# Kernel tuning notes

Measured on AMD Instinct MI355X. Metric: run time of the kernel, lower is better.

Reference implementation:

```python
import jax, jax.numpy as jnp
import numpy as np

B, S, D_MODEL, D_OUT = 4, 4096, 512, 64


def setup_inputs() -> dict:
    key = jax.random.key(0)
    ks = jax.random.split(key, 10)
    query = jax.random.normal(ks[0], (B, S, D_MODEL), dtype=jnp.float32)
    key_t = jax.random.normal(ks[1], (B, S, D_MODEL), dtype=jnp.float32)
    value = jax.random.normal(ks[2], (B, S, D_MODEL), dtype=jnp.float32)
    mask = jax.random.randint(ks[3], (B, S, S), 0, 2, dtype=jnp.int32)
    sc = 1.0 / np.sqrt(D_MODEL)
    Wq = jax.random.uniform(ks[4], (D_MODEL, D_OUT), minval=-sc, maxval=sc, dtype=jnp.float32)
    bq = jnp.zeros((D_OUT,), dtype=jnp.float32)
    Wk = jax.random.uniform(ks[5], (D_MODEL, D_OUT), minval=-sc, maxval=sc, dtype=jnp.float32)
    bk = jnp.zeros((D_OUT,), dtype=jnp.float32)
    Wv = jax.random.uniform(ks[6], (D_MODEL, D_OUT), minval=-sc, maxval=sc, dtype=jnp.float32)
    bv = jnp.zeros((D_OUT,), dtype=jnp.float32)
    return {"query": query, "key": key_t, "value": value, "mask": mask,
            "Wq": Wq, "bq": bq, "Wk": Wk, "bk": bk, "Wv": Wv, "bv": bv}


def reference(query, key, value, mask, Wq, bq, Wk, bk, Wv, bv):
    # Linear projections (single head): [B,S,D_MODEL] @ [D_MODEL,D_OUT] + bias
    q = jnp.einsum('bsd,de->bse', query, Wq) + bq
    k = jnp.einsum('bsd,de->bse', key, Wk) + bk
    v = jnp.einsum('bsd,de->bse', value, Wv) + bv
    dim_k = k.shape[-1]
    scores = jnp.einsum('bqe,bke->bqk', q, k) / jnp.sqrt(jnp.float32(dim_k))  # [B,S,S]
    scores = jnp.where(mask == 0, -jnp.inf, scores)
    weights = jax.nn.softmax(scores, axis=-1)
    # dropout is identity in eval mode / for deterministic reference
    outputs = jnp.einsum('bqk,bke->bqe', weights, v)  # [B,S,D_OUT]
    return outputs
```

## Files before the change

kernel.cpp:

```cpp
#include <hip/hip_runtime.h>
#include <hip/hip_bf16.h>

#define BB 4
#define SS 4096
#define DMODEL 512
#define DOUT 64
#define NKH 2
#define KH (SS / NKH)
#define NIT (KH / 64)

typedef __bf16 bf16_t;
typedef __bf16 bf16x8 __attribute__((ext_vector_type(8)));
typedef float floatx4 __attribute__((ext_vector_type(4)));
typedef unsigned long long u64;
typedef u64 u64x2 __attribute__((ext_vector_type(2)));

__device__ inline void gl_lds16(const void* g, void* l) {
  __builtin_amdgcn_global_load_lds(
      (const __attribute__((address_space(1))) unsigned int*)g,
      (__attribute__((address_space(3))) unsigned int*)l, 16, 0, 0);
}

__global__ __launch_bounds__(256) void wtrans_kernel(
    const float* __restrict__ Wq, const float* __restrict__ Wk,
    const float* __restrict__ Wv, bf16_t* __restrict__ wT) {
  int idx = blockIdx.x * 256 + threadIdx.x;
  int mat = idx >> 12;
  int r   = idx & 4095;
  int e   = r & 63;
  int d0  = (r >> 6) << 3;
  const float* W = (mat == 0) ? Wq : ((mat == 1) ? Wk : Wv);
  bf16_t* dst = wT + (size_t)mat * (DOUT * DMODEL) + (size_t)e * DMODEL + d0;
#pragma unroll
  for (int j = 0; j < 8; ++j) dst[j] = (bf16_t)W[(size_t)(d0 + j) * DOUT + e];
}

__global__ __launch_bounds__(256) void maskpack_kernel(
    const int* __restrict__ mask, u64* __restrict__ bits) {
  const int wid  = (blockIdx.x * 256 + threadIdx.x) >> 6;
  const int lane = threadIdx.x & 63;
  const int* base = mask + (size_t)wid * 1024;
  u64* wbase = bits + (size_t)wid * 16;
#pragma unroll
  for (int c = 0; c < 4; ++c) {
    const int* p = base + c * 256;
    u64 b0 = __ballot(p[lane] != 0);
    u64 b1 = __ballot(p[lane + 64] != 0);
    u64 b2 = __ballot(p[lane + 128] != 0);
    u64 b3 = __ballot(p[lane + 192] != 0);
    u64x2 w01 = {b0, b1}, w23 = {b2, b3};
    if (lane == 0) *(u64x2*)(wbase + c * 4) = w01;
    if (lane == 1) *(u64x2*)(wbase + c * 4 + 2) = w23;
  }
}

__global__ __launch_bounds__(256) void proj_kernel(
    const float* __restrict__ inq, const float* __restrict__ ink,
    const float* __restrict__ inv, const bf16_t* __restrict__ wT,
    const float* __restrict__ bq, const float* __restrict__ bk,
    const float* __restrict__ bv,
    bf16_t* __restrict__ q_ws, bf16_t* __restrict__ k_ws,
    bf16_t* __restrict__ v_wsT) {
  const int mat = blockIdx.x >> 8;
  const int s0  = (blockIdx.x & 255) << 6;
  const int lane = threadIdx.x & 63;
  const int w    = threadIdx.x >> 6;
  const int col  = lane & 15, quad = lane >> 4;

  const float* inp  = (mat == 0) ? inq : ((mat == 1) ? ink : inv);
  const float* bias = (mat == 0) ? bq : ((mat == 1) ? bk : bv);
  const bf16_t* wt  = wT + (size_t)mat * (DOUT * DMODEL);

  const int arow = s0 + w * 16 + col;
  floatx4 acc[4] = {};

  for (int ch = 0; ch < 16; ++ch) {
    const int d0 = ch * 32 + quad * 8;
    float4 a0 = *(const float4*)(inp + (size_t)arow * DMODEL + d0);
    float4 a1 = *(const float4*)(inp + (size_t)arow * DMODEL + d0 + 4);
    bf16x8 af;
    af[0] = (bf16_t)a0.x; af[1] = (bf16_t)a0.y; af[2] = (bf16_t)a0.z; af[3] = (bf16_t)a0.w;
    af[4] = (bf16_t)a1.x; af[5] = (bf16_t)a1.y; af[6] = (bf16_t)a1.z; af[7] = (bf16_t)a1.w;
#pragma unroll
    for (int c = 0; c < 4; ++c) {
      bf16x8 bw = *(const bf16x8*)(wt + (size_t)(c * 16 + col) * DMODEL + d0);
      acc[c] = __builtin_amdgcn_mfma_f32_16x16x32_bf16(af, bw, acc[c], 0, 0, 0);
    }
  }

#pragma unroll
  for (int c = 0; c < 4; ++c) {
    float bcol = bias[c * 16 + col];
#pragma unroll
    for (int r = 0; r < 4; ++r) {
      int row = s0 + w * 16 + quad * 4 + r;
      float v = acc[c][r] + bcol;
      if (mat == 2) {
        int b = row >> 12, sp = row & 4095;
        v_wsT[((size_t)(b * DOUT + c * 16 + col)) * SS + sp] = (bf16_t)v;
      } else {
        bf16_t* dst = (mat == 0) ? q_ws : k_ws;
        dst[(size_t)row * DOUT + c * 16 + col] = (bf16_t)v;
      }
    }
  }
}

__global__ __launch_bounds__(256, 2) void attn_kernel(
    const bf16_t* __restrict__ q_ws, const bf16_t* __restrict__ k_ws,
    const bf16_t* __restrict__ v_wsT, const u64* __restrict__ bits,
    float* __restrict__ O_part, float* __restrict__ l_part) {
  const int bq = blockIdx.x >> 1, kh = blockIdx.x & 1;
  const int b  = bq >> 6;
  const int q0 = (bq & 63) << 6;
  const int kbase = kh * KH;
  const int lane = threadIdx.x & 63;
  const int wi   = threadIdx.x >> 6;
  const int col  = lane & 15, quad = lane >> 4;

  __shared__ __align__(16) bf16_t Kb[2][64 * 64];
  __shared__ __align__(16) bf16_t Vb[2][64 * 64];
  __shared__ __align__(16) bf16_t Pl[4][16][72];

  const int qrowA = q0 + wi * 16 + col;
  const bf16_t* qbase = q_ws + ((size_t)(b * SS) + qrowA) * DOUT + quad * 8;
  const bf16x8 qa0 = *(const bf16x8*)(qbase);
  const bf16x8 qa1 = *(const bf16x8*)(qbase + 32);
  const u64* brow = bits + ((size_t)(b * SS) + qrowA) * (SS / 64);

  const int srow = lane >> 3;
  const int schk = (lane & 7) ^ srow;

  auto stage = [&](int it, int buf) {
    const int k0 = kbase + it * 64;
#pragma unroll
    for (int j = 0; j < 2; ++j) {
      const int i = wi * 2 + j;
      const int r = i * 8 + srow;
      const char* gK = (const char*)(k_ws + ((size_t)(b * SS) + k0 + r) * DOUT) + schk * 16;
      gl_lds16(gK, (char*)(&Kb[buf][0]) + i * 1024);
      const char* gV = (const char*)(v_wsT + ((size_t)(b * DOUT) + r) * SS + k0) + schk * 16;
      gl_lds16(gV, (char*)(&Vb[buf][0]) + i * 1024);
    }
  };

  floatx4 o[4] = {};
  float l_acc = 0.f;
  const bf16_t* prow_r = &Pl[wi][col][quad * 8];

  stage(0, 0);
  u64 bits_cur = brow[kbase >> 6];
  __syncthreads();

  for (int it = 0; it < NIT; ++it) {
    const int buf = it & 1;
    const int itn = (it + 1 < NIT) ? it + 1 : it;

    stage(itn, buf ^ 1);
    u64 bits_nxt = brow[(kbase + itn * 64) >> 6];

    floatx4 sacc[4];
#pragma unroll
    for (int c = 0; c < 4; ++c) {
      const int row = c * 16 + col;
      bf16x8 k0f = *(const bf16x8*)((const char*)&Kb[buf][0] + row * 128 + ((quad ^ (col & 7)) * 16));
      bf16x8 k1f = *(const bf16x8*)((const char*)&Kb[buf][0] + row * 128 + (((4 | quad) ^ (col & 7)) * 16));
      floatx4 z = {};
      z = __builtin_amdgcn_mfma_f32_16x16x32_bf16(qa0, k0f, z, 0, 0, 0);
      z = __builtin_amdgcn_mfma_f32_16x16x32_bf16(qa1, k1f, z, 0, 0, 0);
      sacc[c] = z;
    }

    bf16x8 vc[4][2];
#pragma unroll
    for (int c = 0; c < 4; ++c) {
      const int row = c * 16 + col;
      vc[c][0] = *(const bf16x8*)((const char*)&Vb[buf][0] + row * 128 + ((quad ^ (col & 7)) * 16));
      vc[c][1] = *(const bf16x8*)((const char*)&Vb[buf][0] + row * 128 + (((4 | quad) ^ (col & 7)) * 16));
    }

#pragma unroll
    for (int c = 0; c < 4; ++c)
#pragma unroll
      for (int r = 0; r < 4; ++r)
        Pl[wi][quad * 4 + r][c * 16 + col] = (bf16_t)__expf(sacc[c][r] * 0.125f);

    asm volatile("s_waitcnt lgkmcnt(0)" ::: "memory");

    bf16x8 pa0 = *(const bf16x8*)(prow_r);
    bf16x8 pa1 = *(const bf16x8*)(prow_r + 32);

    unsigned lo32 = (unsigned)bits_cur;
    unsigned hi32 = (unsigned)(bits_cur >> 32);
    unsigned m8a = (lo32 >> (quad * 8)) & 0xffu;
    unsigned m8b = (hi32 >> (quad * 8)) & 0xffu;
    float lp = 0.f;
    bf16x8 pm0, pm1;
#pragma unroll
    for (int j = 0; j < 8; ++j) {
      bf16_t p0 = ((m8a >> j) & 1u) ? pa0[j] : (bf16_t)0.0f;
      bf16_t p1 = ((m8b >> j) & 1u) ? pa1[j] : (bf16_t)0.0f;
      pm0[j] = p0; pm1[j] = p1;
      lp += (float)p0 + (float)p1;
    }
    lp += __shfl_xor(lp, 16);
    lp += __shfl_xor(lp, 32);
    l_acc += lp;

#pragma unroll
    for (int c = 0; c < 4; ++c) {
      o[c] = __builtin_amdgcn_mfma_f32_16x16x32_bf16(pm0, vc[c][0], o[c], 0, 0, 0);
      o[c] = __builtin_amdgcn_mfma_f32_16x16x32_bf16(pm1, vc[c][1], o[c], 0, 0, 0);
    }

    bits_cur = bits_nxt;
    __syncthreads();
  }

  float* Op = O_part + (size_t)blockIdx.x * 64 * 64;
#pragma unroll
  for (int c = 0; c < 4; ++c)
#pragma unroll
    for (int r = 0; r < 4; ++r)
      Op[(wi * 16 + quad * 4 + r) * 64 + c * 16 + col] = o[c][r];
  if (quad == 0) l_part[(size_t)blockIdx.x * 64 + wi * 16 + col] = l_acc;
}

__global__ __launch_bounds__(256) void combine_kernel(
    const float* __restrict__ O_part, const float* __restrict__ l_part,
    float* __restrict__ out) {
  const int idx = blockIdx.x * 256 + threadIdx.x;
  const int base = idx * 4;
  const int row = base >> 6;
  const int c   = base & 63;
  const int t   = row >> 6;
  const int rl  = row & 63;
  const float* p0 = O_part + (((size_t)(t * 2 + 0) * 64 + rl) * 64 + c);
  const float* p1 = O_part + (((size_t)(t * 2 + 1) * 64 + rl) * 64 + c);
  const float inv = 1.0f / (l_part[(size_t)(t * 2) * 64 + rl] +
                            l_part[(size_t)(t * 2 + 1) * 64 + rl]);
  float4 a = *(const float4*)p0;
  float4 b = *(const float4*)p1;
  float4 r4 = {(a.x + b.x) * inv, (a.y + b.y) * inv,
               (a.z + b.z) * inv, (a.w + b.w) * inv};
  *(float4*)(out + base) = r4;
}

extern "C" void kernel_launch(void* const* d_in, const int* in_sizes, int n_in,
                              void* d_out, int out_size, void* d_ws, size_t ws_size,
                              hipStream_t stream) {
  const float* query = (const float*)d_in[0];
  const float* key   = (const float*)d_in[1];
  const float* value = (const float*)d_in[2];
  const int*   mask  = (const int*)d_in[3];
  const float* Wq = (const float*)d_in[4];
  const float* bq = (const float*)d_in[5];
  const float* Wk = (const float*)d_in[6];
  const float* bk = (const float*)d_in[7];
  const float* Wv = (const float*)d_in[8];
  const float* bv = (const float*)d_in[9];
  float* out = (float*)d_out;

  bf16_t* q_ws  = (bf16_t*)d_ws;
  bf16_t* k_ws  = q_ws + (size_t)BB * SS * DOUT;
  bf16_t* v_wsT = k_ws + (size_t)BB * SS * DOUT;
  bf16_t* wT    = v_wsT + (size_t)BB * SS * DOUT;
  float*  O_part = (float*)(wT + 3 * DOUT * DMODEL);
  float*  l_part = O_part + (size_t)512 * 64 * 64;
  u64*    bits   = (u64*)(l_part + 512 * 64);

  hipLaunchKernelGGL(maskpack_kernel, dim3(BB * SS * SS / 1024 / 4), dim3(256), 0, stream,
                     mask, bits);
  hipLaunchKernelGGL(wtrans_kernel, dim3(48), dim3(256), 0, stream, Wq, Wk, Wv, wT);
  hipLaunchKernelGGL(proj_kernel, dim3(768), dim3(256), 0, stream,
                     query, key, value, wT, bq, bk, bv, q_ws, k_ws, v_wsT);
  hipLaunchKernelGGL(attn_kernel, dim3(512), dim3(256), 0, stream,
                     q_ws, k_ws, v_wsT, bits, O_part, l_part);
  hipLaunchKernelGGL(combine_kernel, dim3(1024), dim3(256), 0, stream,
                     O_part, l_part, out);
}
```

Measured before the change: 499.8 us.

## Double query tile per block and split keys four ways

Each attention block now handles 128 query rows (32 per wave) instead of 64, so every K/V tile staged in LDS is reused across twice as many queries. The key range is split into four chunks instead of two, which keeps the grid at 512 blocks, and the combine kernel sums four partials. The MFMA operands are swapped so the score layout lets each lane write a packed bf16x4 of masked probabilities, with masking applied before the LDS write. Register pressure rises because each wave holds twice as many accumulators, and the partial buffers grow.

```diff
diff --git a/kernel.cpp b/kernel.cpp
--- a/kernel.cpp
+++ b/kernel.cpp
@@ -5,11 +5,13 @@
 #define SS 4096
 #define DMODEL 512
 #define DOUT 64
-#define NKH 2
+#define NKH 4
 #define KH (SS / NKH)
-#define NIT (KH / 64)
+#define BK 64
+#define NIT (KH / BK)
 
 typedef __bf16 bf16_t;
+typedef __bf16 bf16x4 __attribute__((ext_vector_type(4)));
 typedef __bf16 bf16x8 __attribute__((ext_vector_type(8)));
 typedef float floatx4 __attribute__((ext_vector_type(4)));
 typedef unsigned long long u64;
@@ -110,46 +112,52 @@
     const bf16_t* __restrict__ q_ws, const bf16_t* __restrict__ k_ws,
     const bf16_t* __restrict__ v_wsT, const u64* __restrict__ bits,
     float* __restrict__ O_part, float* __restrict__ l_part) {
-  const int bq = blockIdx.x >> 1, kh = blockIdx.x & 1;
-  const int b  = bq >> 6;
-  const int q0 = (bq & 63) << 6;
+  const int kh = blockIdx.x & 3;
+  const int qt = (blockIdx.x >> 2) & 31;
+  const int b  = blockIdx.x >> 7;
+  const int q0 = qt * 128;
   const int kbase = kh * KH;
   const int lane = threadIdx.x & 63;
   const int wi   = threadIdx.x >> 6;
   const int col  = lane & 15, quad = lane >> 4;
 
-  __shared__ __align__(16) bf16_t Kb[2][64 * 64];
-  __shared__ __align__(16) bf16_t Vb[2][64 * 64];
-  __shared__ __align__(16) bf16_t Pl[4][16][72];
-
-  const int qrowA = q0 + wi * 16 + col;
-  const bf16_t* qbase = q_ws + ((size_t)(b * SS) + qrowA) * DOUT + quad * 8;
-  const bf16x8 qa0 = *(const bf16x8*)(qbase);
-  const bf16x8 qa1 = *(const bf16x8*)(qbase + 32);
-  const u64* brow = bits + ((size_t)(b * SS) + qrowA) * (SS / 64);
+  __shared__ __align__(16) bf16_t Kb[2][BK * 64];
+  __shared__ __align__(16) bf16_t Vb[2][64 * BK];
+  __shared__ __align__(16) bf16_t Pl[4][32][72];
+
+  bf16x8 qa[2][2];
+#pragma unroll
+  for (int qg = 0; qg < 2; ++qg) {
+    const int qrow = q0 + wi * 32 + qg * 16 + col;
+    const bf16_t* qb = q_ws + ((size_t)(b * SS) + qrow) * DOUT + quad * 8;
+    qa[qg][0] = *(const bf16x8*)(qb);
+    qa[qg][1] = *(const bf16x8*)(qb + 32);
+  }
+  const u64* brow0 = bits + ((size_t)(b * SS) + q0 + wi * 32 + col) * (SS / 64);
+  const u64* brow1 = brow0 + (size_t)16 * (SS / 64);
 
   const int srow = lane >> 3;
   const int schk = (lane & 7) ^ srow;
 
   auto stage = [&](int it, int buf) {
-    const int k0 = kbase + it * 64;
+    const int k0 = kbase + it * BK;
 #pragma unroll
     for (int j = 0; j < 2; ++j) {
       const int i = wi * 2 + j;
       const int r = i * 8 + srow;
-      const char* gK = (const char*)(k_ws + ((size_t)(b * SS) + k0 + r) * DOUT) + schk * 16;
-      gl_lds16(gK, (char*)(&Kb[buf][0]) + i * 1024);
-      const char* gV = (const char*)(v_wsT + ((size_t)(b * DOUT) + r) * SS + k0) + schk * 16;
-      gl_lds16(gV, (char*)(&Vb[buf][0]) + i * 1024);
+      gl_lds16((const char*)(k_ws + ((size_t)(b * SS) + k0 + r) * DOUT) + schk * 16,
+               (char*)(&Kb[buf][0]) + i * 1024);
+      gl_lds16((const char*)(v_wsT + ((size_t)(b * DOUT) + r) * SS + k0) + schk * 16,
+               (char*)(&Vb[buf][0]) + i * 1024);
     }
   };
 
-  floatx4 o[4] = {};
-  float l_acc = 0.f;
-  const bf16_t* prow_r = &Pl[wi][col][quad * 8];
+  floatx4 o[2][4] = {};
+  float lacc[2] = {0.f, 0.f};
 
   stage(0, 0);
-  u64 bits_cur = brow[kbase >> 6];
+  u64 w0c = brow0[kh * NIT + 0];
+  u64 w1c = brow1[kh * NIT + 0];
   __syncthreads();
 
   for (int it = 0; it < NIT; ++it) {
@@ -157,73 +165,84 @@
     const int itn = (it + 1 < NIT) ? it + 1 : it;
 
     stage(itn, buf ^ 1);
-    u64 bits_nxt = brow[(kbase + itn * 64) >> 6];
-
-    floatx4 sacc[4];
+    u64 w0n = brow0[kh * NIT + itn];
+    u64 w1n = brow1[kh * NIT + itn];
+
+    floatx4 st[4][2];
+#pragma unroll
+    for (int kt = 0; kt < 4; ++kt) {
+      const int row = kt * 16 + col;
+      bf16x8 kf0 = *(const bf16x8*)((const char*)&Kb[buf][0] + row * 128 + ((quad ^ (col & 7)) * 16));
+      bf16x8 kf1 = *(const bf16x8*)((const char*)&Kb[buf][0] + row * 128 + (((4 | quad) ^ (col & 7)) * 16));
+#pragma unroll
+      for (int qg = 0; qg < 2; ++qg) {
+        floatx4 z = {};
+        z = __builtin_amdgcn_mfma_f32_16x16x32_bf16(kf0, qa[qg][0], z, 0, 0, 0);
+        z = __builtin_amdgcn_mfma_f32_16x16x32_bf16(kf1, qa[qg][1], z, 0, 0, 0);
+        st[kt][qg] = z;
+      }
+    }
+
+    bf16x8 vf[4][2];
 #pragma unroll
     for (int c = 0; c < 4; ++c) {
       const int row = c * 16 + col;
-      bf16x8 k0f = *(const bf16x8*)((const char*)&Kb[buf][0] + row * 128 + ((quad ^ (col & 7)) * 16));
-      bf16x8 k1f = *(const bf16x8*)((const char*)&Kb[buf][0] + row * 128 + (((4 | quad) ^ (col & 7)) * 16));
-      floatx4 z = {};
-      z = __builtin_amdgcn_mfma_f32_16x16x32_bf16(qa0, k0f, z, 0, 0, 0);
-      z = __builtin_amdgcn_mfma_f32_16x16x32_bf16(qa1, k1f, z, 0, 0, 0);
-      sacc[c] = z;
-    }
-
-    bf16x8 vc[4][2];
-#pragma unroll
-    for (int c = 0; c < 4; ++c) {
-      const int row = c * 16 + col;
-      vc[c][0] = *(const bf16x8*)((const char*)&Vb[buf][0] + row * 128 + ((quad ^ (col & 7)) * 16));
-      vc[c][1] = *(const bf16x8*)((const char*)&Vb[buf][0] + row * 128 + (((4 | quad) ^ (col & 7)) * 16));
-    }
-
+      vf[c][0] = *(const bf16x8*)((const char*)&Vb[buf][0] + row * 128 + ((quad ^ (col & 7)) * 16));
+      vf[c][1] = *(const bf16x8*)((const char*)&Vb[buf][0] + row * 128 + (((4 | quad) ^ (col & 7)) * 16));
+    }
+
+#pragma unroll
+    for (int qg = 0; qg < 2; ++qg) {
+      const u64 w = qg ? w1c : w0c;
+#pragma unroll
+      for (int kt = 0; kt < 4; ++kt) {
+        const unsigned nib = (unsigned)(w >> (kt * 16 + quad * 4)) & 0xfu;
+        float p[4];
+#pragma unroll
+        for (int r = 0; r < 4; ++r) {
+          float e = __expf(st[kt][qg][r] * 0.125f);
+          p[r] = (nib >> r & 1u) ? e : 0.0f;
+          lacc[qg] += p[r];
+        }
+        bf16x4 pk = {(bf16_t)p[0], (bf16_t)p[1], (bf16_t)p[2], (bf16_t)p[3]};
+        *(bf16x4*)(&Pl[wi][qg * 16 + col][kt * 16 + quad * 4]) = pk;
+      }
+    }
+
+    asm volatile("s_waitcnt lgkmcnt(0)" ::: "memory");
+
+    bf16x8 pf[2][2];
+#pragma unroll
+    for (int qg = 0; qg < 2; ++qg) {
+      pf[qg][0] = *(const bf16x8*)(&Pl[wi][qg * 16 + col][quad * 8]);
+      pf[qg][1] = *(const bf16x8*)(&Pl[wi][qg * 16 + col][32 + quad * 8]);
+    }
 #pragma unroll
     for (int c = 0; c < 4; ++c)
 #pragma unroll
-      for (int r = 0; r < 4; ++r)
-        Pl[wi][quad * 4 + r][c * 16 + col] = (bf16_t)__expf(sacc[c][r] * 0.125f);
-
-    asm volatile("s_waitcnt lgkmcnt(0)" ::: "memory");
-
-    bf16x8 pa0 = *(const bf16x8*)(prow_r);
-    bf16x8 pa1 = *(const bf16x8*)(prow_r + 32);
-
-    unsigned lo32 = (unsigned)bits_cur;
-    unsigned hi32 = (unsigned)(bits_cur >> 32);
-    unsigned m8a = (lo32 >> (quad * 8)) & 0xffu;
-    unsigned m8b = (hi32 >> (quad * 8)) & 0xffu;
-    float lp = 0.f;
-    bf16x8 pm0, pm1;
-#pragma unroll
-    for (int j = 0; j < 8; ++j) {
-      bf16_t p0 = ((m8a >> j) & 1u) ? pa0[j] : (bf16_t)0.0f;
-      bf16_t p1 = ((m8b >> j) & 1u) ? pa1[j] : (bf16_t)0.0f;
-      pm0[j] = p0; pm1[j] = p1;
-      lp += (float)p0 + (float)p1;
-    }
+      for (int qg = 0; qg < 2; ++qg) {
+        o[qg][c] = __builtin_amdgcn_mfma_f32_16x16x32_bf16(vf[c][0], pf[qg][0], o[qg][c], 0, 0, 0);
+        o[qg][c] = __builtin_amdgcn_mfma_f32_16x16x32_bf16(vf[c][1], pf[qg][1], o[qg][c], 0, 0, 0);
+      }
+
+    w0c = w0n; w1c = w1n;
+    __syncthreads();
+  }
+
+  float* Op = O_part + (size_t)blockIdx.x * 128 * 64;
+#pragma unroll
+  for (int qg = 0; qg < 2; ++qg) {
+    float lp = lacc[qg];
     lp += __shfl_xor(lp, 16);
     lp += __shfl_xor(lp, 32);
-    l_acc += lp;
-
+    const int rl = wi * 32 + qg * 16 + col;
+    if (quad == 0) l_part[(size_t)blockIdx.x * 128 + rl] = lp;
 #pragma unroll
     for (int c = 0; c < 4; ++c) {
-      o[c] = __builtin_amdgcn_mfma_f32_16x16x32_bf16(pm0, vc[c][0], o[c], 0, 0, 0);
-      o[c] = __builtin_amdgcn_mfma_f32_16x16x32_bf16(pm1, vc[c][1], o[c], 0, 0, 0);
-    }
-
-    bits_cur = bits_nxt;
-    __syncthreads();
-  }
-
-  float* Op = O_part + (size_t)blockIdx.x * 64 * 64;
-#pragma unroll
-  for (int c = 0; c < 4; ++c)
-#pragma unroll
-    for (int r = 0; r < 4; ++r)
-      Op[(wi * 16 + quad * 4 + r) * 64 + c * 16 + col] = o[c][r];
-  if (quad == 0) l_part[(size_t)blockIdx.x * 64 + wi * 16 + col] = l_acc;
+      float4 v = {o[qg][c][0], o[qg][c][1], o[qg][c][2], o[qg][c][3]};
+      *(float4*)(Op + (size_t)rl * 64 + c * 16 + quad * 4) = v;
+    }
+  }
 }
 
 __global__ __launch_bounds__(256) void combine_kernel(
@@ -233,16 +252,19 @@
   const int base = idx * 4;
   const int row = base >> 6;
   const int c   = base & 63;
-  const int t   = row >> 6;
-  const int rl  = row & 63;
-  const float* p0 = O_part + (((size_t)(t * 2 + 0) * 64 + rl) * 64 + c);
-  const float* p1 = O_part + (((size_t)(t * 2 + 1) * 64 + rl) * 64 + c);
-  const float inv = 1.0f / (l_part[(size_t)(t * 2) * 64 + rl] +
-                            l_part[(size_t)(t * 2 + 1) * 64 + rl]);
-  float4 a = *(const float4*)p0;
-  float4 b = *(const float4*)p1;
-  float4 r4 = {(a.x + b.x) * inv, (a.y + b.y) * inv,
-               (a.z + b.z) * inv, (a.w + b.w) * inv};
+  const int t   = row >> 7;
+  const int rl  = row & 127;
+  float4 acc = {0.f, 0.f, 0.f, 0.f};
+  float lsum = 0.f;
+#pragma unroll
+  for (int kh = 0; kh < NKH; ++kh) {
+    const size_t blk = (size_t)(t * NKH + kh);
+    float4 a = *(const float4*)(O_part + (blk * 128 + rl) * 64 + c);
+    acc.x += a.x; acc.y += a.y; acc.z += a.z; acc.w += a.w;
+    lsum += l_part[blk * 128 + rl];
+  }
+  const float inv = 1.0f / lsum;
+  float4 r4 = {acc.x * inv, acc.y * inv, acc.z * inv, acc.w * inv};
   *(float4*)(out + base) = r4;
 }
 
@@ -266,15 +288,15 @@
   bf16_t* v_wsT = k_ws + (size_t)BB * SS * DOUT;
   bf16_t* wT    = v_wsT + (size_t)BB * SS * DOUT;
   float*  O_part = (float*)(wT + 3 * DOUT * DMODEL);
-  float*  l_part = O_part + (size_t)512 * 64 * 64;
-  u64*    bits   = (u64*)(l_part + 512 * 64);
+  float*  l_part = O_part + (size_t)512 * 128 * 64;
+  u64*    bits   = (u64*)(l_part + 512 * 128);
 
   hipLaunchKernelGGL(maskpack_kernel, dim3(BB * SS * SS / 1024 / 4), dim3(256), 0, stream,
                      mask, bits);
   hipLaunchKernelGGL(wtrans_kernel, dim3(48), dim3(256), 0, stream, Wq, Wk, Wv, wT);
   hipLaunchKernelGGL(proj_kernel, dim3(768), dim3(256), 0, stream,
                      query, key, value, wT, bq, bk, bv, q_ws, k_ws, v_wsT);
-  hipLaunchKernelGGL(attn_kernel, dim3(512), dim3(256), 0, stream,
+  hipLaunchKernelGGL(attn_kernel, dim3(BB * 32 * NKH), dim3(256), 0, stream,
                      q_ws, k_ws, v_wsT, bits, O_part, l_part);
   hipLaunchKernelGGL(combine_kernel, dim3(1024), dim3(256), 0, stream,
                      O_part, l_part, out);
```

Measured after the change: 486.1 us. 2.7% less time.
